# Performance work log

Hardware: AMD Instinct MI355X
Metric: run time of the kernel (lower is better)

Reference implementation:

```python
import jax, jax.numpy as jnp
import numpy as np

B, N, EDGES = 16, 50000, 1600000
CLAMP_MIN, CLAMP_MAX = -10.0, 10.0
EPS = 1e-6


def setup_inputs() -> dict:
    key = jax.random.key(0)
    ks = jax.random.split(key, 8)
    return {
        "chem_influence": jax.random.normal(ks[0], (B, N), dtype=jnp.float32),
        "E": jax.random.normal(ks[1], (B, N), dtype=jnp.float32),
        "o_pre": jax.random.uniform(ks[2], (B, N), dtype=jnp.float32),
        "w": jax.random.normal(ks[3], (EDGES,), dtype=jnp.float32),
        "threshold": jax.random.uniform(ks[4], (N,), dtype=jnp.float32),
        "decay": jax.random.uniform(ks[5], (N,), dtype=jnp.float32),
        "src": jax.random.randint(ks[6], (EDGES,), 0, N, dtype=jnp.int32),
        "dst": jax.random.randint(ks[7], (EDGES,), 0, N, dtype=jnp.int32),
    }


def reference(chem_influence, E, o_pre, w, threshold, decay, src, dst):
    # Gap-junction currents: gather, sign-compare, weighted scatter-add.
    Oj = o_pre[:, src]                      # (B, EDGES) presynaptic outputs
    En = E[:, dst]                          # (B, EDGES) postsynaptic internal states
    sgn = jnp.where(Oj >= En, 1.0, -1.0)
    contrib = Oj * w * sgn                  # (B, EDGES)
    gj_sum = jnp.zeros_like(chem_influence).at[:, dst].add(contrib)  # (B, N)

    # Neuron dynamics (eqs 10, 11).
    S = jnp.clip(E + chem_influence + gj_sum, CLAMP_MIN, CLAMP_MAX)
    gt = S > threshold                      # broadcast (N,) over (B, N)
    mask = (~gt) & (jnp.abs(S - E) <= EPS)
    new_o = jax.nn.relu(S - threshold)
    new_e = jnp.where(gt, new_o, jnp.where(mask, E - decay, S))
    return (new_o, new_e)
```

## Files before the change

kernel.cpp:

```cpp
#include <hip/hip_runtime.h>

#define BATCH 16
#define NNODES 50000
#define NEDGES 1600000
#define BN (BATCH * NNODES)
#define EPB 8192
#define NBLK 196
#define BSZ 128
#define NBINS 391
#define CAPE 4992
#define CLAMP_LO -10.0f
#define CLAMP_HI 10.0f
#define EPS_V 1e-6f

__global__ void transpose_kernel(const float* __restrict__ o_pre,
                                 const float* __restrict__ E,
                                 float* __restrict__ o_t,
                                 float* __restrict__ E_t) {
    int t = blockIdx.x * blockDim.x + threadIdx.x;
    if (t >= NNODES) return;
    float v[BATCH], u[BATCH];
#pragma unroll
    for (int b = 0; b < BATCH; ++b) {
        v[b] = o_pre[b * NNODES + t];
        u[b] = E[b * NNODES + t];
    }
    float4* op = (float4*)(o_t + (size_t)t * BATCH);
    float4* ep = (float4*)(E_t + (size_t)t * BATCH);
#pragma unroll
    for (int k = 0; k < 4; ++k) {
        op[k] = make_float4(v[4 * k], v[4 * k + 1], v[4 * k + 2], v[4 * k + 3]);
        ep[k] = make_float4(u[4 * k], u[4 * k + 1], u[4 * k + 2], u[4 * k + 3]);
    }
}

__global__ void hist_kernel(const int* __restrict__ dst,
                            int* __restrict__ hist) {
    __shared__ int lh[NBINS];
    int t = threadIdx.x;
    for (int i = t; i < NBINS; i += 256) lh[i] = 0;
    __syncthreads();
    int eb = blockIdx.x * EPB;
#pragma unroll
    for (int j = 0; j < 32; ++j) {
        int e = eb + j * 256 + t;
        if (e < NEDGES) atomicAdd(&lh[dst[e] >> 7], 1);
    }
    __syncthreads();
    for (int i = t; i < NBINS; i += 256) hist[i * NBLK + blockIdx.x] = lh[i];
}

__global__ void scanA_kernel(int* __restrict__ hist, int* __restrict__ totals) {
    __shared__ int sm[256];
    int k = blockIdx.x, t = threadIdx.x;
    int v = (t < NBLK) ? hist[k * NBLK + t] : 0;
    sm[t] = v;
    __syncthreads();
    for (int off = 1; off < 256; off <<= 1) {
        int a = (t >= off) ? sm[t - off] : 0;
        __syncthreads();
        sm[t] += a;
        __syncthreads();
    }
    if (t < NBLK) hist[k * NBLK + t] = sm[t] - v;
    if (t == 0) totals[k] = sm[NBLK - 1];
}

__global__ void scanB_kernel(const int* __restrict__ totals,
                             int* __restrict__ base) {
    __shared__ int sm[512];
    int t = threadIdx.x;
    int v = (t < NBINS) ? totals[t] : 0;
    sm[t] = v;
    __syncthreads();
    for (int off = 1; off < 512; off <<= 1) {
        int a = (t >= off) ? sm[t - off] : 0;
        __syncthreads();
        sm[t] += a;
        __syncthreads();
    }
    if (t < NBINS) base[t] = sm[t] - v;
    if (t == 0) base[NBINS] = sm[NBINS - 1];
}

__global__ void scatterA_kernel(const int* __restrict__ src,
                                const int* __restrict__ dst,
                                const float* __restrict__ w,
                                const int* __restrict__ hist,
                                const int* __restrict__ base,
                                uint2* __restrict__ binned) {
    __shared__ int cur[NBINS];
    int t = threadIdx.x;
    for (int i = t; i < NBINS; i += 256)
        cur[i] = base[i] + hist[i * NBLK + blockIdx.x];
    __syncthreads();
    int eb = blockIdx.x * EPB;
#pragma unroll
    for (int j = 0; j < 32; ++j) {
        int e = eb + j * 256 + t;
        if (e < NEDGES) {
            int d = dst[e];
            int pos = atomicAdd(&cur[d >> 7], 1);
            binned[pos] = make_uint2((unsigned)src[e] | ((unsigned)(d & 127) << 16),
                                     __float_as_uint(w[e]));
        }
    }
}

__global__ __launch_bounds__(512) void bin_gather2(
    const float* __restrict__ o_t,
    const float* __restrict__ E_t,
    const float* __restrict__ chem,
    const float* __restrict__ threshold,
    const float* __restrict__ decay,
    const int* __restrict__ base,
    const uint2* __restrict__ binned,
    float* __restrict__ out_o,
    float* __restrict__ out_e) {
    __shared__ int   cnt_l[BSZ];
    __shared__ int   offs[BSZ + 1];
    __shared__ int   sc[BSZ];
    __shared__ uint2 eb[CAPE];

    const int k = blockIdx.x, tid = threadIdx.x;
    const int node0 = k * BSZ;
    const int nn = (NNODES - node0 < BSZ) ? (NNODES - node0) : BSZ;
    const int s0 = base[k], s1 = base[k + 1];

    if (tid < BSZ) cnt_l[tid] = 0;
    __syncthreads();
    for (int i = s0 + tid; i < s1; i += 512)
        atomicAdd(&cnt_l[(binned[i].x >> 16) & 127], 1);
    __syncthreads();

    if (tid < BSZ) sc[tid] = cnt_l[tid];
    __syncthreads();
    for (int o = 1; o < BSZ; o <<= 1) {
        int v = (tid >= o && tid < BSZ) ? sc[tid - o] : 0;
        __syncthreads();
        if (tid < BSZ) sc[tid] += v;
        __syncthreads();
    }
    if (tid < BSZ) {
        int ex = sc[tid] - cnt_l[tid];
        offs[tid] = ex;
        cnt_l[tid] = ex;
    }
    if (tid == 0) offs[BSZ] = s1 - s0;
    __syncthreads();

    for (int i = s0 + tid; i < s1; i += 512) {
        uint2 p = binned[i];
        int pos = atomicAdd(&cnt_l[(p.x >> 16) & 127], 1);
        if (pos < CAPE) eb[pos] = p;
    }
    __syncthreads();

    for (int t = tid; t < nn * 4; t += 512) {
        int n = t >> 2;
        int q = (t & 3) * 4;
        int gn = node0 + n;
        int e0 = offs[n], e1 = offs[n + 1];
        float4 en = *(const float4*)(E_t + (size_t)gn * BATCH + q);
        float4 acc = make_float4(0.f, 0.f, 0.f, 0.f);
        for (int i = e0; i < e1; ++i) {
            uint2 p = eb[i];
            float wv = __uint_as_float(p.y);
            int s = (int)(p.x & 0xFFFFu);
            float4 oj = *(const float4*)(o_t + (size_t)s * BATCH + q);
            acc.x += (oj.x >= en.x) ? oj.x * wv : -oj.x * wv;
            acc.y += (oj.y >= en.y) ? oj.y * wv : -oj.y * wv;
            acc.z += (oj.z >= en.z) ? oj.z * wv : -oj.z * wv;
            acc.w += (oj.w >= en.w) ? oj.w * wv : -oj.w * wv;
        }
        float th = threshold[gn];
        float dc = decay[gn];
        float ev[4] = {en.x, en.y, en.z, en.w};
        float av[4] = {acc.x, acc.y, acc.z, acc.w};
#pragma unroll
        for (int j = 0; j < 4; ++j) {
            int b = q + j;
            float e = ev[j];
            float S = e + chem[b * NNODES + gn] + av[j];
            S = fminf(fmaxf(S, CLAMP_LO), CLAMP_HI);
            float no = fmaxf(S - th, 0.0f);
            float ne;
            if (S > th) ne = no;
            else if (fabsf(S - e) <= EPS_V) ne = e - dc;
            else ne = S;
            out_o[b * NNODES + gn] = no;
            out_e[b * NNODES + gn] = ne;
        }
    }
}

__global__ void edge_scatter_dev(const float* __restrict__ o_pre, const float* __restrict__ E,
                                 const float* __restrict__ w, const int* __restrict__ src,
                                 const int* __restrict__ dst, float* __restrict__ gj) {
    int e = blockIdx.x * blockDim.x + threadIdx.x;
    if (e >= NEDGES) return;
    int s = src[e];
    int d = dst[e];
    float wv = w[e];
#pragma unroll
    for (int b = 0; b < BATCH; ++b) {
        float oj = o_pre[b * NNODES + s];
        float en = E[b * NNODES + d];
        atomicAdd(&gj[b * NNODES + d], (oj >= en) ? oj * wv : -oj * wv);
    }
}

__global__ void finalize_dev(const float* __restrict__ chem, const float* __restrict__ E,
                             const float* __restrict__ threshold, const float* __restrict__ decay,
                             float* __restrict__ out_o, float* __restrict__ out_e_gj) {
    int i = blockIdx.x * blockDim.x + threadIdx.x;
    if (i >= BN) return;
    int n = i % NNODES;
    float e = E[i];
    float S = e + chem[i] + out_e_gj[i];
    S = fminf(fmaxf(S, CLAMP_LO), CLAMP_HI);
    float th = threshold[n];
    float no = fmaxf(S - th, 0.0f);
    float ne;
    if (S > th) ne = no;
    else if (fabsf(S - e) <= EPS_V) ne = e - decay[n];
    else ne = S;
    out_o[i] = no;
    out_e_gj[i] = ne;
}

extern "C" void kernel_launch(void* const* d_in, const int* in_sizes, int n_in,
                              void* d_out, int out_size, void* d_ws, size_t ws_size,
                              hipStream_t stream) {
    const float* chem      = (const float*)d_in[0];
    const float* E         = (const float*)d_in[1];
    const float* o_pre     = (const float*)d_in[2];
    const float* w         = (const float*)d_in[3];
    const float* threshold = (const float*)d_in[4];
    const float* decay     = (const float*)d_in[5];
    const int*   src       = (const int*)d_in[6];
    const int*   dst       = (const int*)d_in[7];

    float* out_o = (float*)d_out;
    float* out_e = (float*)d_out + BN;

    const size_t OT_OFF  = 0;
    const size_t ET_OFF  = 3200000;
    const size_t BIN_OFF = 6400000;
    const size_t H_OFF   = 19200000;
    const size_t TOT_OFF = 19506560;
    const size_t BAS_OFF = 19508128;
    const size_t need    = BAS_OFF + (size_t)(NBINS + 1) * sizeof(int);

    if (ws_size >= need) {
        char* ws = (char*)d_ws;
        float* o_t    = (float*)(ws + OT_OFF);
        float* E_t    = (float*)(ws + ET_OFF);
        uint2* binned = (uint2*)(ws + BIN_OFF);
        int*   hist   = (int*)(ws + H_OFF);
        int*   totals = (int*)(ws + TOT_OFF);
        int*   base   = (int*)(ws + BAS_OFF);

        transpose_kernel<<<(NNODES + 255) / 256, 256, 0, stream>>>(o_pre, E, o_t, E_t);
        hist_kernel<<<NBLK, 256, 0, stream>>>(dst, hist);
        scanA_kernel<<<NBINS, 256, 0, stream>>>(hist, totals);
        scanB_kernel<<<1, 512, 0, stream>>>(totals, base);
        scatterA_kernel<<<NBLK, 256, 0, stream>>>(src, dst, w, hist, base, binned);
        bin_gather2<<<NBINS, 512, 0, stream>>>(o_t, E_t, chem, threshold, decay,
                                               base, binned, out_o, out_e);
    } else {
        hipMemsetAsync(out_e, 0, (size_t)BN * sizeof(float), stream);
        edge_scatter_dev<<<(NEDGES + 255) / 256, 256, 0, stream>>>(o_pre, E, w, src, dst, out_e);
        finalize_dev<<<(BN + 255) / 256, 256, 0, stream>>>(chem, E, threshold, decay, out_o, out_e);
    }
}
```

Before: 150.9 us.

## Fuse transpose into histogram kernel, drop global scan with fixed-capacity bins, vectorize edge loads

```diff
diff --git a/kernel.cpp b/kernel.cpp
--- a/kernel.cpp
+++ b/kernel.cpp
@@ -4,8 +4,8 @@
 #define NNODES 50000
 #define NEDGES 1600000
 #define BN (BATCH * NNODES)
+#define NBLK 196
 #define EPB 8192
-#define NBLK 196
 #define BSZ 128
 #define NBINS 391
 #define CAPE 4992
@@ -13,41 +13,49 @@
 #define CLAMP_HI 10.0f
 #define EPS_V 1e-6f
 
-__global__ void transpose_kernel(const float* __restrict__ o_pre,
+__global__ void prep_hist_kernel(const float* __restrict__ o_pre,
                                  const float* __restrict__ E,
+                                 const int* __restrict__ dst,
                                  float* __restrict__ o_t,
-                                 float* __restrict__ E_t) {
-    int t = blockIdx.x * blockDim.x + threadIdx.x;
-    if (t >= NNODES) return;
-    float v[BATCH], u[BATCH];
-#pragma unroll
-    for (int b = 0; b < BATCH; ++b) {
-        v[b] = o_pre[b * NNODES + t];
-        u[b] = E[b * NNODES + t];
-    }
-    float4* op = (float4*)(o_t + (size_t)t * BATCH);
-    float4* ep = (float4*)(E_t + (size_t)t * BATCH);
-#pragma unroll
-    for (int k = 0; k < 4; ++k) {
-        op[k] = make_float4(v[4 * k], v[4 * k + 1], v[4 * k + 2], v[4 * k + 3]);
-        ep[k] = make_float4(u[4 * k], u[4 * k + 1], u[4 * k + 2], u[4 * k + 3]);
-    }
-}
-
-__global__ void hist_kernel(const int* __restrict__ dst,
-                            int* __restrict__ hist) {
+                                 float* __restrict__ E_t,
+                                 int* __restrict__ hist) {
     __shared__ int lh[NBINS];
-    int t = threadIdx.x;
-    for (int i = t; i < NBINS; i += 256) lh[i] = 0;
-    __syncthreads();
-    int eb = blockIdx.x * EPB;
-#pragma unroll
-    for (int j = 0; j < 32; ++j) {
-        int e = eb + j * 256 + t;
-        if (e < NEDGES) atomicAdd(&lh[dst[e] >> 7], 1);
-    }
-    __syncthreads();
-    for (int i = t; i < NBINS; i += 256) hist[i * NBLK + blockIdx.x] = lh[i];
+    const int tid = threadIdx.x, bid = blockIdx.x;
+    for (int i = tid; i < NBINS; i += 256) lh[i] = 0;
+
+    int t = bid * 256 + tid;
+    if (t < NNODES) {
+        float v[BATCH], u[BATCH];
+#pragma unroll
+        for (int b = 0; b < BATCH; ++b) {
+            v[b] = o_pre[b * NNODES + t];
+            u[b] = E[b * NNODES + t];
+        }
+        float4* op = (float4*)(o_t + (size_t)t * BATCH);
+        float4* ep = (float4*)(E_t + (size_t)t * BATCH);
+#pragma unroll
+        for (int k = 0; k < 4; ++k) {
+            op[k] = make_float4(v[4 * k], v[4 * k + 1], v[4 * k + 2], v[4 * k + 3]);
+            ep[k] = make_float4(u[4 * k], u[4 * k + 1], u[4 * k + 2], u[4 * k + 3]);
+        }
+    }
+    __syncthreads();
+
+    const int4* dst4 = (const int4*)dst;
+    const int e4base = bid * (EPB / 4);
+#pragma unroll
+    for (int j = 0; j < 8; ++j) {
+        int i4 = e4base + j * 256 + tid;
+        if (i4 * 4 < NEDGES) {
+            int4 d4 = dst4[i4];
+            atomicAdd(&lh[d4.x >> 7], 1);
+            atomicAdd(&lh[d4.y >> 7], 1);
+            atomicAdd(&lh[d4.z >> 7], 1);
+            atomicAdd(&lh[d4.w >> 7], 1);
+        }
+    }
+    __syncthreads();
+    for (int i = tid; i < NBINS; i += 256) hist[i * NBLK + bid] = lh[i];
 }
 
 __global__ void scanA_kernel(int* __restrict__ hist, int* __restrict__ totals) {
@@ -63,46 +71,43 @@
         __syncthreads();
     }
     if (t < NBLK) hist[k * NBLK + t] = sm[t] - v;
-    if (t == 0) totals[k] = sm[NBLK - 1];
-}
-
-__global__ void scanB_kernel(const int* __restrict__ totals,
-                             int* __restrict__ base) {
-    __shared__ int sm[512];
-    int t = threadIdx.x;
-    int v = (t < NBINS) ? totals[t] : 0;
-    sm[t] = v;
-    __syncthreads();
-    for (int off = 1; off < 512; off <<= 1) {
-        int a = (t >= off) ? sm[t - off] : 0;
-        __syncthreads();
-        sm[t] += a;
-        __syncthreads();
-    }
-    if (t < NBINS) base[t] = sm[t] - v;
-    if (t == 0) base[NBINS] = sm[NBINS - 1];
+    if (t == 0) totals[k] = sm[255];
 }
 
 __global__ void scatterA_kernel(const int* __restrict__ src,
                                 const int* __restrict__ dst,
                                 const float* __restrict__ w,
                                 const int* __restrict__ hist,
-                                const int* __restrict__ base,
                                 uint2* __restrict__ binned) {
     __shared__ int cur[NBINS];
-    int t = threadIdx.x;
-    for (int i = t; i < NBINS; i += 256)
-        cur[i] = base[i] + hist[i * NBLK + blockIdx.x];
-    __syncthreads();
-    int eb = blockIdx.x * EPB;
-#pragma unroll
-    for (int j = 0; j < 32; ++j) {
-        int e = eb + j * 256 + t;
-        if (e < NEDGES) {
-            int d = dst[e];
-            int pos = atomicAdd(&cur[d >> 7], 1);
-            binned[pos] = make_uint2((unsigned)src[e] | ((unsigned)(d & 127) << 16),
-                                     __float_as_uint(w[e]));
+    const int tid = threadIdx.x, bid = blockIdx.x;
+    for (int i = tid; i < NBINS; i += 256)
+        cur[i] = i * CAPE + hist[i * NBLK + bid];
+    __syncthreads();
+    const int4*   dst4 = (const int4*)dst;
+    const int4*   src4 = (const int4*)src;
+    const float4* w4   = (const float4*)w;
+    const int e4base = bid * (EPB / 4);
+#pragma unroll
+    for (int j = 0; j < 8; ++j) {
+        int i4 = e4base + j * 256 + tid;
+        if (i4 * 4 < NEDGES) {
+            int4 d4 = dst4[i4];
+            int4 s4 = src4[i4];
+            float4 ww = w4[i4];
+            int dd[4] = {d4.x, d4.y, d4.z, d4.w};
+            int ss[4] = {s4.x, s4.y, s4.z, s4.w};
+            float wv[4] = {ww.x, ww.y, ww.z, ww.w};
+#pragma unroll
+            for (int m = 0; m < 4; ++m) {
+                int d = dd[m];
+                int bin = d >> 7;
+                int pos = atomicAdd(&cur[bin], 1);
+                if (pos < (bin + 1) * CAPE)
+                    binned[pos] = make_uint2(
+                        (unsigned)ss[m] | ((unsigned)(d & 127) << 16),
+                        __float_as_uint(wv[m]));
+            }
         }
     }
 }
@@ -113,7 +118,7 @@
     const float* __restrict__ chem,
     const float* __restrict__ threshold,
     const float* __restrict__ decay,
-    const int* __restrict__ base,
+    const int* __restrict__ totals,
     const uint2* __restrict__ binned,
     float* __restrict__ out_o,
     float* __restrict__ out_e) {
@@ -125,7 +130,10 @@
     const int k = blockIdx.x, tid = threadIdx.x;
     const int node0 = k * BSZ;
     const int nn = (NNODES - node0 < BSZ) ? (NNODES - node0) : BSZ;
-    const int s0 = base[k], s1 = base[k + 1];
+    const int s0 = k * CAPE;
+    int cnt = totals[k];
+    if (cnt > CAPE) cnt = CAPE;
+    const int s1 = s0 + cnt;
 
     if (tid < BSZ) cnt_l[tid] = 0;
     __syncthreads();
@@ -146,7 +154,7 @@
         offs[tid] = ex;
         cnt_l[tid] = ex;
     }
-    if (tid == 0) offs[BSZ] = s1 - s0;
+    if (tid == 0) offs[BSZ] = cnt;
     __syncthreads();
 
     for (int i = s0 + tid; i < s1; i += 512) {
@@ -247,10 +255,9 @@
     const size_t OT_OFF  = 0;
     const size_t ET_OFF  = 3200000;
     const size_t BIN_OFF = 6400000;
-    const size_t H_OFF   = 19200000;
-    const size_t TOT_OFF = 19506560;
-    const size_t BAS_OFF = 19508128;
-    const size_t need    = BAS_OFF + (size_t)(NBINS + 1) * sizeof(int);
+    const size_t H_OFF   = 22014976;
+    const size_t TOT_OFF = 22321536;
+    const size_t need    = TOT_OFF + (size_t)NBINS * sizeof(int);
 
     if (ws_size >= need) {
         char* ws = (char*)d_ws;
@@ -259,15 +266,12 @@
         uint2* binned = (uint2*)(ws + BIN_OFF);
         int*   hist   = (int*)(ws + H_OFF);
         int*   totals = (int*)(ws + TOT_OFF);
-        int*   base   = (int*)(ws + BAS_OFF);
-
-        transpose_kernel<<<(NNODES + 255) / 256, 256, 0, stream>>>(o_pre, E, o_t, E_t);
-        hist_kernel<<<NBLK, 256, 0, stream>>>(dst, hist);
+
+        prep_hist_kernel<<<NBLK, 256, 0, stream>>>(o_pre, E, dst, o_t, E_t, hist);
         scanA_kernel<<<NBINS, 256, 0, stream>>>(hist, totals);
-        scanB_kernel<<<1, 512, 0, stream>>>(totals, base);
-        scatterA_kernel<<<NBLK, 256, 0, stream>>>(src, dst, w, hist, base, binned);
+        scatterA_kernel<<<NBLK, 256, 0, stream>>>(src, dst, w, hist, binned);
         bin_gather2<<<NBINS, 512, 0, stream>>>(o_t, E_t, chem, threshold, decay,
-                                               base, binned, out_o, out_e);
+                                               totals, binned, out_o, out_e);
     } else {
         hipMemsetAsync(out_e, 0, (size_t)BN * sizeof(float), stream);
         edge_scatter_dev<<<(NEDGES + 255) / 256, 256, 0, stream>>>(o_pre, E, w, src, dst, out_e);
```

Measured after the change: 132.3 us. -12.3%, faster.
